# Performance work log

Measured on AMD Instinct MI355X. Metric: run time of the kernel, lower is better.

## Reference

```python
import jax, jax.numpy as jnp
import numpy as np

B, N, H = 1024, 128, 128
T = 2 * N  # max_steps default: 2 * n_nodes
NEG = -1e9
TEMPERATURE = 1.0


def setup_inputs() -> dict:
    key = jax.random.key(0)
    ks = jax.random.split(key, 12)
    coords = jax.random.uniform(ks[0], (B, N, 2), dtype=jnp.float32)
    demands = jax.random.uniform(ks[1], (B, N), dtype=jnp.float32) * 0.3
    demands = demands.at[:, 0].set(0.0)  # depot has zero demand
    capacities = jnp.ones((B,), jnp.float32)
    s = 0.1
    return dict(
        coords=coords, demands=demands, capacities=capacities,
        W_emb=jax.random.normal(ks[2], (3, H), jnp.float32) * s, b_emb=jnp.zeros((H,), jnp.float32),
        Wq=jax.random.normal(ks[3], (H, H), jnp.float32) * s, bq=jnp.zeros((H,), jnp.float32),
        Wk=jax.random.normal(ks[4], (H, H), jnp.float32) * s, bk=jnp.zeros((H,), jnp.float32),
        Wv=jax.random.normal(ks[5], (H, H), jnp.float32) * s, bv=jnp.zeros((H,), jnp.float32),
        Wp1=jax.random.normal(ks[6], (2 * H, H), jnp.float32) * s, bp1=jnp.zeros((H,), jnp.float32),
        Wp2=jax.random.normal(ks[7], (H, 1), jnp.float32) * s, bp2=jnp.zeros((1,), jnp.float32),
    )


def _forward(coords, demands, capacities, W_emb, b_emb, Wq, bq, Wk, bk, Wv, bv, Wp1, bp1, Wp2, bp2):
    # --- encoder: single self-attention pass (done once, outside the decode loop) ---
    nf = jnp.concatenate([coords, demands[..., None]], axis=-1)           # [B,N,3]
    emb = nf @ W_emb + b_emb                                               # [B,N,H]
    Q = emb @ Wq + bq
    K = emb @ Wk + bk
    V = emb @ Wv + bv
    attn = jax.nn.softmax(jnp.einsum('bnh,bmh->bnm', Q, K) / jnp.sqrt(jnp.float32(H)), axis=-1)
    att_emb = jnp.einsum('bnm,bmh->bnh', attn, V)                          # [B,N,H]
    idx = jnp.arange(N)

    def step(carry, key_t):
        visited, rem_cap, at_depot, done = carry
        # done when all customers visited and currently at depot
        done = done | (visited[:, 1:].all(-1) & at_depot)
        # context = masked mean of unvisited node embeddings (zeros if none)
        unvis = (~visited).astype(att_emb.dtype)                           # [B,N]
        cnt = unvis.sum(-1, keepdims=True)
        ctx = jnp.einsum('bn,bnh->bh', unvis, att_emb) / jnp.maximum(cnt, 1.0)
        pin = jnp.concatenate([att_emb, jnp.broadcast_to(ctx[:, None, :], att_emb.shape)], -1)
        sc = (jax.nn.relu(pin @ Wp1 + bp1) @ Wp2 + bp2)[..., 0]            # [B,N]
        # feasibility mask: visited, over-capacity, depot-if-at-depot
        mask = visited | (demands > rem_cap[:, None])
        mask = mask.at[:, 0].set(mask[:, 0] | at_depot)
        all_masked = mask.all(-1)
        # if everything masked and not at depot -> allow returning to depot
        mask = mask.at[:, 0].set(mask[:, 0] & ~(all_masked & ~at_depot))
        # if everything masked and at depot -> done
        done = done | (all_masked & at_depot)
        # keep logits finite for done rows (their log-prob is zeroed below)
        mask = mask.at[:, 0].set(mask[:, 0] & ~done)
        logits = jnp.where(mask, NEG, sc) / TEMPERATURE
        lp = jax.nn.log_softmax(logits, axis=-1)
        action = jax.random.categorical(key_t, logits)                     # multinomial sampling
        sel = jnp.take_along_axis(lp, action[:, None], 1)[:, 0]
        sel = jnp.where(done, 0.0, sel)
        action = jnp.where(done, 0, action)
        is_depot = action == 0
        upd = ~done
        visited = visited | ((idx[None, :] == action[:, None]) & (upd & ~is_depot)[:, None])
        d_taken = jnp.take_along_axis(demands, action[:, None], 1)[:, 0]
        rem_cap = jnp.where(upd, jnp.where(is_depot, capacities, rem_cap - d_taken), rem_cap)
        at_depot = jnp.where(upd, is_depot, at_depot)
        return (visited, rem_cap, at_depot, done), (action, sel)

    keys = jax.random.split(jax.random.key(42), T)
    init = (jnp.zeros((B, N), bool), capacities, jnp.ones((B,), bool), jnp.zeros((B,), bool))
    _, (actions, lps) = jax.lax.scan(step, init, keys)
    return actions.T, lps.sum(0)  # routes [B,T] (0-padded when done), combined log-probs [B]


def reference(coords, demands, capacities, W_emb, b_emb, Wq, bq, Wk, bk, Wv, bv, Wp1, bp1, Wp2, bp2):
    return _forward(coords, demands, capacities, W_emb, b_emb, Wq, bq, Wk, bk, Wv, bv, Wp1, bp1, Wp2, bp2)
```

## Files before the change

### kernel.cpp

```cpp
#include <hip/hip_runtime.h>
#include <stdint.h>
#include <stddef.h>


#define NEGV (-1e9f)

__device__ __forceinline__ uint32_t rotl32(uint32_t v, int d) { return (v << d) | (v >> (32 - d)); }

__device__ __forceinline__ void threefry2x32(uint32_t k0, uint32_t k1, uint32_t c0, uint32_t c1,
                                             uint32_t& o0, uint32_t& o1) {
  uint32_t k2 = k0 ^ k1 ^ 0x1BD11BDAu;
  uint32_t x0 = c0 + k0, x1 = c1 + k1;
  x0 += x1; x1 = rotl32(x1, 13); x1 ^= x0;
  x0 += x1; x1 = rotl32(x1, 15); x1 ^= x0;
  x0 += x1; x1 = rotl32(x1, 26); x1 ^= x0;
  x0 += x1; x1 = rotl32(x1, 6);  x1 ^= x0;
  x0 += k1; x1 += k2 + 1u;
  x0 += x1; x1 = rotl32(x1, 17); x1 ^= x0;
  x0 += x1; x1 = rotl32(x1, 29); x1 ^= x0;
  x0 += x1; x1 = rotl32(x1, 16); x1 ^= x0;
  x0 += x1; x1 = rotl32(x1, 24); x1 ^= x0;
  x0 += k2; x1 += k0 + 2u;
  x0 += x1; x1 = rotl32(x1, 13); x1 ^= x0;
  x0 += x1; x1 = rotl32(x1, 15); x1 ^= x0;
  x0 += x1; x1 = rotl32(x1, 26); x1 ^= x0;
  x0 += x1; x1 = rotl32(x1, 6);  x1 ^= x0;
  x0 += k0; x1 += k1 + 3u;
  x0 += x1; x1 = rotl32(x1, 17); x1 ^= x0;
  x0 += x1; x1 = rotl32(x1, 29); x1 ^= x0;
  x0 += x1; x1 = rotl32(x1, 16); x1 ^= x0;
  x0 += x1; x1 = rotl32(x1, 24); x1 ^= x0;
  x0 += k1; x1 += k2 + 4u;
  x0 += x1; x1 = rotl32(x1, 13); x1 ^= x0;
  x0 += x1; x1 = rotl32(x1, 15); x1 ^= x0;
  x0 += x1; x1 = rotl32(x1, 26); x1 ^= x0;
  x0 += x1; x1 = rotl32(x1, 6);  x1 ^= x0;
  x0 += k2; x1 += k0 + 5u;
  o0 = x0; o1 = x1;
}

__device__ __forceinline__ float gumbel_from(uint32_t kA, uint32_t kB, uint32_t idx) {
  uint32_t o0, o1;
  threefry2x32(kA, kB, 0u, idx, o0, o1);
  uint32_t bits = o0 ^ o1;
  uint32_t mb = bits >> 9;
  float u = (mb == 0u) ? 1.17549435e-38f : (float)mb * 1.1920928955078125e-07f;
  return -logf(-logf(u));
}

__device__ void mm128(const float* Alds, float* wst,
                      const float* __restrict__ W, const float* __restrict__ bias,
                      float* outg, int t) {
  int wv = t >> 6, lane = t & 63;
  int j0 = lane * 2;
  float b0 = 0.f, b1 = 0.f;
  if (bias) { b0 = bias[j0]; b1 = bias[j0 + 1]; }
  int r0 = wv * 32;
  float acc0[4][8], acc1[4][8];
#pragma unroll
  for (int g = 0; g < 4; ++g)
#pragma unroll
    for (int r = 0; r < 8; ++r) { acc0[g][r] = b0; acc1[g][r] = b1; }
  for (int ks = 0; ks < 128; ks += 16) {
    __syncthreads();
    for (int i = t; i < 2048; i += 256) wst[i] = W[ks * 128 + i];
    __syncthreads();
#pragma unroll
    for (int k4 = 0; k4 < 16; k4 += 4) {
      float2 w[4];
#pragma unroll
      for (int kk = 0; kk < 4; ++kk) w[kk] = *(const float2*)&wst[(k4 + kk) * 128 + j0];
#pragma unroll
      for (int g = 0; g < 4; ++g)
#pragma unroll
        for (int r = 0; r < 8; ++r) {
          float4 a = *(const float4*)&Alds[(r0 + g * 8 + r) * 128 + ks + k4];
          acc0[g][r] = fmaf(a.x, w[0].x, acc0[g][r]); acc1[g][r] = fmaf(a.x, w[0].y, acc1[g][r]);
          acc0[g][r] = fmaf(a.y, w[1].x, acc0[g][r]); acc1[g][r] = fmaf(a.y, w[1].y, acc1[g][r]);
          acc0[g][r] = fmaf(a.z, w[2].x, acc0[g][r]); acc1[g][r] = fmaf(a.z, w[2].y, acc1[g][r]);
          acc0[g][r] = fmaf(a.w, w[3].x, acc0[g][r]); acc1[g][r] = fmaf(a.w, w[3].y, acc1[g][r]);
        }
    }
  }
#pragma unroll
  for (int g = 0; g < 4; ++g)
#pragma unroll
    for (int r = 0; r < 8; ++r) {
      int n = r0 + g * 8 + r;
      float2 o; o.x = acc0[g][r]; o.y = acc1[g][r];
      *(float2*)&outg[n * 128 + j0] = o;
    }
}

__global__ __launch_bounds__(256, 2) void pn_e1(
    const float* __restrict__ coords, const float* __restrict__ demands,
    const float* __restrict__ W_emb, const float* __restrict__ b_emb,
    const float* __restrict__ Wq, const float* __restrict__ bq,
    const float* __restrict__ Wk, const float* __restrict__ bk,
    const float* __restrict__ Wv, const float* __restrict__ bv,
    float* Qo, float* Ko, float* Vo) {
  __shared__ float emb[128 * 128];
  __shared__ float wst[16 * 128];
  __shared__ float nfx[128], nfy[128], nfd[128];
  int b = blockIdx.x, t = threadIdx.x;
  if (t < 128) {
    float2 c = ((const float2*)coords)[b * 128 + t];
    nfx[t] = c.x; nfy[t] = c.y; nfd[t] = demands[b * 128 + t];
  }
  __syncthreads();
  {
    int h = t >> 1, n0 = (t & 1) * 64;
    float w0 = W_emb[h], w1 = W_emb[128 + h], w2 = W_emb[256 + h], be = b_emb[h];
    for (int n = n0; n < n0 + 64; ++n) {
      float e = nfx[n] * w0;
      e = fmaf(nfy[n], w1, e);
      e = fmaf(nfd[n], w2, e);
      e = e + be;
      emb[n * 128 + h] = e;
    }
  }
  __syncthreads();
  mm128(emb, wst, Wq, bq, Qo + (size_t)b * 16384, t);
  mm128(emb, wst, Wk, bk, Ko + (size_t)b * 16384, t);
  mm128(emb, wst, Wv, bv, Vo + (size_t)b * 16384, t);
}

__global__ __launch_bounds__(256, 2) void pn_e2(
    const float* Qg, const float* __restrict__ Kg, const float* __restrict__ Vg, float* atto) {
  __shared__ float Ks[128 * 132];
  __shared__ float qb[4 * 512];
  int b = blockIdx.x, t = threadIdx.x;
  int wv = t >> 6, lane = t & 63;
  const float sden = sqrtf(128.0f);
  for (int i = t; i < 16384; i += 256) {
    int m = i >> 7, k = i & 127;
    Ks[m * 132 + k] = Kg[(size_t)b * 16384 + i];
  }
  __syncthreads();
  const float* Vb = Vg + (size_t)b * 16384;
  for (int pass = 0; pass < 8; ++pass) {
    int nb = pass * 16 + wv * 4;
    for (int i = lane; i < 512; i += 64) qb[wv * 512 + i] = Qg[(size_t)b * 16384 + nb * 128 + i];
    __syncthreads();
    float s0[4] = {0.f, 0.f, 0.f, 0.f}, s1[4] = {0.f, 0.f, 0.f, 0.f};
    for (int k = 0; k < 128; k += 4) {
      float4 ka = *(const float4*)&Ks[lane * 132 + k];
      float4 kb = *(const float4*)&Ks[(lane + 64) * 132 + k];
#pragma unroll
      for (int r = 0; r < 4; ++r) {
        float4 q = *(const float4*)&qb[wv * 512 + r * 128 + k];
        s0[r] = fmaf(q.x, ka.x, s0[r]); s0[r] = fmaf(q.y, ka.y, s0[r]);
        s0[r] = fmaf(q.z, ka.z, s0[r]); s0[r] = fmaf(q.w, ka.w, s0[r]);
        s1[r] = fmaf(q.x, kb.x, s1[r]); s1[r] = fmaf(q.y, kb.y, s1[r]);
        s1[r] = fmaf(q.z, kb.z, s1[r]); s1[r] = fmaf(q.w, kb.w, s1[r]);
      }
    }
    float p0[4], p1[4];
#pragma unroll
    for (int r = 0; r < 4; ++r) {
      float a0 = s0[r] / sden, a1 = s1[r] / sden;
      float mx = fmaxf(a0, a1);
#pragma unroll
      for (int off = 1; off < 64; off <<= 1) mx = fmaxf(mx, __shfl_xor(mx, off));
      float e0 = expf(a0 - mx), e1 = expf(a1 - mx);
      float sm = e0 + e1;
#pragma unroll
      for (int off = 1; off < 64; off <<= 1) sm += __shfl_xor(sm, off);
      p0[r] = e0 / sm; p1[r] = e1 / sm;
    }
#pragma unroll
    for (int r = 0; r < 4; ++r) {
      qb[wv * 512 + r * 128 + lane] = p0[r];
      qb[wv * 512 + r * 128 + lane + 64] = p1[r];
    }
    __syncthreads();
    float o0[4] = {0.f, 0.f, 0.f, 0.f}, o1[4] = {0.f, 0.f, 0.f, 0.f};
    for (int m4 = 0; m4 < 128; m4 += 4) {
      float4 p[4];
#pragma unroll
      for (int r = 0; r < 4; ++r) p[r] = *(const float4*)&qb[wv * 512 + r * 128 + m4];
#pragma unroll
      for (int mm = 0; mm < 4; ++mm) {
        float v0 = Vb[(m4 + mm) * 128 + lane];
        float v1 = Vb[(m4 + mm) * 128 + lane + 64];
#pragma unroll
        for (int r = 0; r < 4; ++r) {
          float pv = (mm == 0) ? p[r].x : (mm == 1) ? p[r].y : (mm == 2) ? p[r].z : p[r].w;
          o0[r] = fmaf(pv, v0, o0[r]);
          o1[r] = fmaf(pv, v1, o1[r]);
        }
      }
    }
#pragma unroll
    for (int r = 0; r < 4; ++r) {
      atto[(size_t)b * 16384 + (nb + r) * 128 + lane] = o0[r];
      atto[(size_t)b * 16384 + (nb + r) * 128 + lane + 64] = o1[r];
    }
    __syncthreads();
  }
}

__global__ __launch_bounds__(256, 2) void pn_e3(
    const float* attg, const float* __restrict__ Wp1,
    const float* __restrict__ bp1, float* A1o, float* Po) {
  __shared__ float att[128 * 128];
  __shared__ float wst[16 * 128];
  int b = blockIdx.x, t = threadIdx.x;
  for (int i = t; i < 16384; i += 256) att[i] = attg[(size_t)b * 16384 + i];
  __syncthreads();
  mm128(att, wst, Wp1, bp1, A1o + (size_t)b * 16384, t);
  mm128(att, wst, Wp1 + 16384, (const float*)0, Po + (size_t)b * 16384, t);
}

__global__ __launch_bounds__(256, 2) void pn_decode(
    const float* __restrict__ A1g, const float* __restrict__ Pg,
    const float* __restrict__ demands, const float* __restrict__ caps,
    const float* __restrict__ Wp2, const float* __restrict__ bp2, float* out) {
  __shared__ __align__(16) float Pt[128 * 132];
  __shared__ __align__(16) float c1[128];
  __shared__ float scv[128];
  __shared__ float dem[128];
  __shared__ int acts[256];
  __shared__ uint32_t keyA[256], keyB[256];

  int b = blockIdx.x, t = threadIdx.x;
  int lane = t & 63;
  { uint32_t o0, o1; threefry2x32(0u, 42u, 0u, (uint32_t)t, o0, o1); keyA[t] = o0; keyB[t] = o1; }
  for (int i = t; i < 16384; i += 256) {
    int n = i >> 7, h = i & 127;
    Pt[h * 132 + n] = Pg[(size_t)b * 16384 + i];
  }
  int nrow = t >> 1, half = t & 1;
  float a1r[64], w2r[64];
  {
    const float4* asrc = (const float4*)(A1g + (size_t)b * 16384 + nrow * 128 + half * 64);
    const float4* wsrc = (const float4*)(Wp2 + half * 64);
#pragma unroll
    for (int j = 0; j < 16; ++j) {
      float4 v = asrc[j];
      a1r[4 * j] = v.x; a1r[4 * j + 1] = v.y; a1r[4 * j + 2] = v.z; a1r[4 * j + 3] = v.w;
      float4 w = wsrc[j];
      w2r[4 * j] = w.x; w2r[4 * j + 1] = w.y; w2r[4 * j + 2] = w.z; w2r[4 * j + 3] = w.w;
    }
  }
  if (t < 128) dem[t] = demands[b * 128 + t];
  acts[t] = 0;
  float capv = caps[b];
  float bp2v = bp2[0];
  float dem0 = demands[b * 128 + lane];
  float dem1 = demands[b * 128 + lane + 64];
  unsigned long long vism0 = 0ull, vism1 = 0ull;
  float rc = capv, lps = 0.f;
  int at = 1, done = 0, vc = 0;
  __syncthreads();

  for (int step = 0; step < 256; ++step) {
    if (t < 128) {
      float cnt = fmaxf((float)(128 - vc), 1.f);
      const float* pr = &Pt[t * 132];
      float acc = 0.f;
#pragma unroll
      for (int q = 0; q < 32; ++q) {
        float4 p = *(const float4*)&pr[q * 4];
        unsigned long long w = (q < 16) ? vism0 : vism1;
        int base = (q * 4) & 63;
        acc += ((w >> base) & 1ull) ? 0.f : p.x;
        acc += ((w >> (base + 1)) & 1ull) ? 0.f : p.y;
        acc += ((w >> (base + 2)) & 1ull) ? 0.f : p.z;
        acc += ((w >> (base + 3)) & 1ull) ? 0.f : p.w;
      }
      c1[t] = acc / cnt;
    }
    __syncthreads();

    {
      const float* crow = &c1[half * 64];
      float acc = 0.f;
#pragma unroll
      for (int q = 0; q < 16; ++q) {
        float4 c4 = *(const float4*)&crow[q * 4];
        float x;
        x = a1r[4 * q] + c4.x;     x = fmaxf(x, 0.f); acc = fmaf(x, w2r[4 * q], acc);
        x = a1r[4 * q + 1] + c4.y; x = fmaxf(x, 0.f); acc = fmaf(x, w2r[4 * q + 1], acc);
        x = a1r[4 * q + 2] + c4.z; x = fmaxf(x, 0.f); acc = fmaf(x, w2r[4 * q + 2], acc);
        x = a1r[4 * q + 3] + c4.w; x = fmaxf(x, 0.f); acc = fmaf(x, w2r[4 * q + 3], acc);
      }
      float other = __shfl_xor(acc, 1);
      if (half == 0) scv[nrow] = (acc + other) + bp2v;
    }
    __syncthreads();

    {
      uint32_t kA = keyA[step], kB = keyB[step];
      float g0 = gumbel_from(kA, kB, (uint32_t)(b * 128 + lane));
      float g1 = gumbel_from(kA, kB, (uint32_t)(b * 128 + lane + 64));
      bool mk0 = (lane == 0) ? (at != 0)
                             : ((((vism0 >> lane) & 1ull) != 0ull) || (dem0 > rc));
      bool mk1 = (((vism1 >> lane) & 1ull) != 0ull) || (dem1 > rc);
      unsigned long long bl0 = __ballot(mk0 ? 1 : 0);
      unsigned long long bl1 = __ballot(mk1 ? 1 : 0);
      int d = done;
      if (vc == 127 && at) d = 1;
      bool am = (bl0 == ~0ull) && (bl1 == ~0ull);
      if (am && at) d = 1;
      if (lane == 0) mk0 = (at && !d);
      float sc0 = scv[lane], sc1 = scv[lane + 64];
      float lg0 = mk0 ? NEGV : sc0;
      float lg1 = mk1 ? NEGV : sc1;
      float v0g = g0 + lg0, v1g = g1 + lg1;
      float v; int idx;
      if (v1g > v0g) { v = v1g; idx = lane + 64; } else { v = v0g; idx = lane; }
      float mx = fmaxf(lg0, lg1);
#pragma unroll
      for (int off = 1; off < 64; off <<= 1) {
        float ov = __shfl_xor(v, off);
        int oi = __shfl_xor(idx, off);
        if (ov > v || (ov == v && oi < idx)) { v = ov; idx = oi; }
        mx = fmaxf(mx, __shfl_xor(mx, off));
      }
      float e = expf(lg0 - mx) + expf(lg1 - mx);
#pragma unroll
      for (int off = 1; off < 64; off <<= 1) e += __shfl_xor(e, off);
      int a = d ? 0 : idx;
      float sellg = scv[idx];
      float sel = d ? 0.f : ((sellg - mx) - logf(e));
      lps += sel;
      if (t == 0) acts[step] = a;
      if (!d) {
        if (a == 0) { rc = capv; at = 1; }
        else {
          rc = rc - dem[a];
          at = 0; vc = vc + 1;
          if (a < 64) vism0 |= (1ull << a); else vism1 |= (1ull << (a - 64));
        }
      }
      done = d;
    }
    if (done) break;
    __syncthreads();
  }

  __syncthreads();
  out[(size_t)b * 256 + t] = (float)acts[t];
  if (t == 0) out[(size_t)1024 * 256 + b] = lps;
}

extern "C" void kernel_launch(void* const* d_in, const int* in_sizes, int n_in,
                              void* d_out, int out_size, void* d_ws, size_t ws_size,
                              hipStream_t stream) {
  (void)in_sizes; (void)n_in; (void)out_size; (void)ws_size;
  const float* coords  = (const float*)d_in[0];
  const float* demands = (const float*)d_in[1];
  const float* caps    = (const float*)d_in[2];
  const float* W_emb   = (const float*)d_in[3];
  const float* b_emb   = (const float*)d_in[4];
  const float* Wq      = (const float*)d_in[5];
  const float* bq      = (const float*)d_in[6];
  const float* Wk      = (const float*)d_in[7];
  const float* bk      = (const float*)d_in[8];
  const float* Wv      = (const float*)d_in[9];
  const float* bv      = (const float*)d_in[10];
  const float* Wp1     = (const float*)d_in[11];
  const float* bp1     = (const float*)d_in[12];
  const float* Wp2     = (const float*)d_in[13];
  const float* bp2     = (const float*)d_in[14];

  float* ws = (float*)d_ws;
  const size_t R = (size_t)1024 * 128 * 128;
  float* R0 = ws;
  float* R1 = ws + R;
  float* R2 = ws + 2 * R;

  pn_e1<<<1024, 256, 0, stream>>>(coords, demands, W_emb, b_emb, Wq, bq, Wk, bk, Wv, bv, R0, R1, R2);
  pn_e2<<<1024, 256, 0, stream>>>(R0, R1, R2, R0);
  pn_e3<<<1024, 256, 0, stream>>>(R0, Wp1, bp1, R0, R1);
  pn_decode<<<1024, 256, 0, stream>>>(R0, R1, demands, caps, Wp2, bp2, (float*)d_out);
}
```

Before: 2.308 ms.

## Precompute Gumbel noise one step ahead on idle waves and use float unvisited mask

Gumbel noise for the next step is now generated by waves 2-3 while wave 0 computes the context sum, and stored in a triple-buffered shared array instead of being computed inline on the critical path. The context reduction moves to a single wave using a shared float mask with FMAs instead of per-bit selects. The softmax normaliser is computed only by wave 0, and the trailing barrier is removed. The removed barrier and the 3-slot rotation rely on the remaining two barriers for ordering, which adds a risk of shared-memory races. Putting the whole context sum on one wave also lengthens that phase.

```diff
diff --git a/kernel.cpp b/kernel.cpp
--- a/kernel.cpp
+++ b/kernel.cpp
@@ -218,13 +218,15 @@
     const float* __restrict__ Wp2, const float* __restrict__ bp2, float* out) {
   __shared__ __align__(16) float Pt[128 * 132];
   __shared__ __align__(16) float c1[128];
+  __shared__ __align__(16) float mf[128];
   __shared__ float scv[128];
   __shared__ float dem[128];
+  __shared__ float gv[3][128];
   __shared__ int acts[256];
   __shared__ uint32_t keyA[256], keyB[256];
 
   int b = blockIdx.x, t = threadIdx.x;
-  int lane = t & 63;
+  int wave = t >> 6, lane = t & 63;
   { uint32_t o0, o1; threefry2x32(0u, 42u, 0u, (uint32_t)t, o0, o1); keyA[t] = o0; keyB[t] = o1; }
   for (int i = t; i < 16384; i += 256) {
     int n = i >> 7, h = i & 127;
@@ -243,7 +245,7 @@
       w2r[4 * j] = w.x; w2r[4 * j + 1] = w.y; w2r[4 * j + 2] = w.z; w2r[4 * j + 3] = w.w;
     }
   }
-  if (t < 128) dem[t] = demands[b * 128 + t];
+  if (t < 128) { dem[t] = demands[b * 128 + t]; mf[t] = 1.0f; }
   acts[t] = 0;
   float capv = caps[b];
   float bp2v = bp2[0];
@@ -253,23 +255,31 @@
   float rc = capv, lps = 0.f;
   int at = 1, done = 0, vc = 0;
   __syncthreads();
-
+  if (t >= 128) gv[0][t - 128] = gumbel_from(keyA[0], keyB[0], (uint32_t)(b * 128 + (t - 128)));
+
+  int rslot = 0;
   for (int step = 0; step < 256; ++step) {
-    if (t < 128) {
+    int wslot = rslot + 1; if (wslot == 3) wslot = 0;
+    if (wave == 0) {
       float cnt = fmaxf((float)(128 - vc), 1.f);
-      const float* pr = &Pt[t * 132];
-      float acc = 0.f;
-#pragma unroll
+      const float* p0 = &Pt[lane * 132];
+      const float* p1 = &Pt[(lane + 64) * 132];
+      float acc0 = 0.f, acc1 = 0.f;
+#pragma unroll 8
       for (int q = 0; q < 32; ++q) {
-        float4 p = *(const float4*)&pr[q * 4];
-        unsigned long long w = (q < 16) ? vism0 : vism1;
-        int base = (q * 4) & 63;
-        acc += ((w >> base) & 1ull) ? 0.f : p.x;
-        acc += ((w >> (base + 1)) & 1ull) ? 0.f : p.y;
-        acc += ((w >> (base + 2)) & 1ull) ? 0.f : p.z;
-        acc += ((w >> (base + 3)) & 1ull) ? 0.f : p.w;
-      }
-      c1[t] = acc / cnt;
+        float4 m4 = *(const float4*)&mf[q * 4];
+        float4 x0 = *(const float4*)&p0[q * 4];
+        float4 x1 = *(const float4*)&p1[q * 4];
+        acc0 = fmaf(x0.x, m4.x, acc0); acc0 = fmaf(x0.y, m4.y, acc0);
+        acc0 = fmaf(x0.z, m4.z, acc0); acc0 = fmaf(x0.w, m4.w, acc0);
+        acc1 = fmaf(x1.x, m4.x, acc1); acc1 = fmaf(x1.y, m4.y, acc1);
+        acc1 = fmaf(x1.z, m4.z, acc1); acc1 = fmaf(x1.w, m4.w, acc1);
+      }
+      c1[lane] = acc0 / cnt;
+      c1[lane + 64] = acc1 / cnt;
+    } else if (t >= 128 && step < 255) {
+      int n = t - 128;
+      gv[wslot][n] = gumbel_from(keyA[step + 1], keyB[step + 1], (uint32_t)(b * 128 + n));
     }
     __syncthreads();
 
@@ -291,9 +301,7 @@
     __syncthreads();
 
     {
-      uint32_t kA = keyA[step], kB = keyB[step];
-      float g0 = gumbel_from(kA, kB, (uint32_t)(b * 128 + lane));
-      float g1 = gumbel_from(kA, kB, (uint32_t)(b * 128 + lane + 64));
+      float g0 = gv[rslot][lane], g1 = gv[rslot][lane + 64];
       bool mk0 = (lane == 0) ? (at != 0)
                              : ((((vism0 >> lane) & 1ull) != 0ull) || (dem0 > rc));
       bool mk1 = (((vism1 >> lane) & 1ull) != 0ull) || (dem1 > rc);
@@ -301,8 +309,7 @@
       unsigned long long bl1 = __ballot(mk1 ? 1 : 0);
       int d = done;
       if (vc == 127 && at) d = 1;
-      bool am = (bl0 == ~0ull) && (bl1 == ~0ull);
-      if (am && at) d = 1;
+      if ((bl0 == ~0ull) && (bl1 == ~0ull) && at) d = 1;
       if (lane == 0) mk0 = (at && !d);
       float sc0 = scv[lane], sc1 = scv[lane + 64];
       float lg0 = mk0 ? NEGV : sc0;
@@ -318,14 +325,17 @@
         if (ov > v || (ov == v && oi < idx)) { v = ov; idx = oi; }
         mx = fmaxf(mx, __shfl_xor(mx, off));
       }
-      float e = expf(lg0 - mx) + expf(lg1 - mx);
-#pragma unroll
-      for (int off = 1; off < 64; off <<= 1) e += __shfl_xor(e, off);
       int a = d ? 0 : idx;
-      float sellg = scv[idx];
-      float sel = d ? 0.f : ((sellg - mx) - logf(e));
-      lps += sel;
-      if (t == 0) acts[step] = a;
+      if (wave == 0) {
+        float e = expf(lg0 - mx) + expf(lg1 - mx);
+#pragma unroll
+        for (int off = 1; off < 64; off <<= 1) e += __shfl_xor(e, off);
+        if (lane == 0) {
+          float sel = d ? 0.f : ((scv[idx] - mx) - logf(e));
+          lps += sel;
+          acts[step] = a;
+        }
+      }
       if (!d) {
         if (a == 0) { rc = capv; at = 1; }
         else {
@@ -335,9 +345,13 @@
         }
       }
       done = d;
-    }
+      if (wave == 0) {
+        mf[lane]      = (((vism0 >> lane) & 1ull) != 0ull) ? 0.f : 1.f;
+        mf[lane + 64] = (((vism1 >> lane) & 1ull) != 0ull) ? 0.f : 1.f;
+      }
+    }
+    rslot = wslot;
     if (done) break;
-    __syncthreads();
   }
 
   __syncthreads();
```

After: 2.310 ms. About the same (+0.1%).
